# Kernel tuning notes

Hardware: AMD Instinct MI355X
Metric: run time of the kernel (lower is better)

Reference implementation:

```python
import jax, jax.numpy as jnp
import numpy as np

WIN = 32            # window_size
LOW_TH, HIGH_TH = 5.0, 15.0  # density_thresholds


def _prelu(x, a):
    return jnp.where(x >= 0, x, a * x)


def _hist_density(x):
    B, _, N = x.shape
    i, q = x[:, 0], x[:, 1]
    scale = WIN / 4.0  # bins over range [-2, 2]
    ii = jnp.clip(jnp.floor((i + 2.0) * scale).astype(jnp.int32), 0, WIN - 1)
    qq = jnp.clip(jnp.floor((q + 2.0) * scale).astype(jnp.int32), 0, WIN - 1)
    valid = (i >= -2.0) & (i <= 2.0) & (q >= -2.0) & (q <= 2.0)
    boff = jnp.arange(B, dtype=jnp.int32)[:, None] * (WIN * WIN)
    flat = (boff + ii * WIN + qq).reshape(-1)
    H = jax.ops.segment_sum(valid.astype(jnp.float32).reshape(-1), flat,
                            num_segments=B * WIN * WIN).reshape(B, WIN, WIN)
    low = (H <= LOW_TH).astype(jnp.float32)
    med = ((H > LOW_TH) & (H <= HIGH_TH)).astype(jnp.float32)
    high = (H > HIGH_TH).astype(jnp.float32)
    return jnp.stack([high, med, low], axis=1)


def _conv(x, w, b, p):
    y = jax.lax.conv_general_dilated(x, w, (1, 1), [(p, p), (p, p)],
                                     dimension_numbers=('NCHW', 'OIHW', 'NCHW'))
    return y + b[None, :, None, None]


def _avgpool2(x):
    B, C, H, W = x.shape
    return x.reshape(B, C, H // 2, 2, W // 2, 2).mean(axis=(3, 5))


def setup_inputs():
    key = jax.random.key(0)
    ks = jax.random.split(key, 8)
    B, N = 4096, 1024
    x = jax.random.normal(ks[0], (B, 2, N), jnp.float32)

    def w(k, shape, fan_in):
        return jax.random.normal(k, shape, jnp.float32) * (1.0 / np.sqrt(fan_in))

    return {
        'x': x,
        'cw1': w(ks[1], (32, 3, 3, 3), 3 * 9),   'cb1': jnp.zeros(32, jnp.float32),  'a1': jnp.float32(0.25),
        'cw2': w(ks[2], (64, 32, 3, 3), 32 * 9),  'cb2': jnp.zeros(64, jnp.float32),  'a2': jnp.float32(0.25),
        'cw3': w(ks[3], (128, 64, 5, 5), 64 * 25),'cb3': jnp.zeros(128, jnp.float32), 'a3': jnp.float32(0.25),
        'fw1': w(ks[4], (256, 128 * 4 * 4), 128 * 4 * 4), 'fb1': jnp.zeros(256, jnp.float32), 'a4': jnp.float32(0.25),
        'fw2': w(ks[5], (128, 256), 256), 'fb2': jnp.zeros(128, jnp.float32),
    }


def reference(x, cw1, cb1, a1, cw2, cb2, a2, cw3, cb3, a3, fw1, fb1, a4, fw2, fb2):
    d = _hist_density(x)                              # [B, 3, 32, 32]
    h = _avgpool2(_prelu(_conv(d, cw1, cb1, 1), a1))  # [B, 32, 16, 16]
    h = _avgpool2(_prelu(_conv(h, cw2, cb2, 1), a2))  # [B, 64, 8, 8]
    h = _avgpool2(_prelu(_conv(h, cw3, cb3, 2), a3))  # [B, 128, 4, 4]
    # AdaptiveAvgPool2d((4,4)) is identity on 4x4; Dropout is identity in eval
    f = h.reshape(h.shape[0], -1)                     # [B, 2048]
    f = _prelu(f @ fw1.T + fb1, a4)                   # [B, 256]
    return f @ fw2.T + fb2                            # [B, 128]
```

## Files before the change

kernel.cpp:

```cpp
#include <hip/hip_runtime.h>
#include <hip/hip_bf16.h>
#include <cstdint>
#include <cstddef>

typedef short short8 __attribute__((ext_vector_type(8)));
typedef float f32x4 __attribute__((ext_vector_type(4)));
typedef float f32x16 __attribute__((ext_vector_type(16)));
typedef unsigned short u16x4 __attribute__((ext_vector_type(4)));

__device__ inline unsigned short f2b(float f) {
    union { __hip_bfloat16 h; unsigned short u; } cv;
    cv.h = __float2bfloat16(f);
    return cv.u;
}
__device__ inline float b2f(unsigned short u) {
    union { __hip_bfloat16 h; unsigned short u; } cv;
    cv.u = u;
    return __bfloat162float(cv.h);
}
__device__ inline float prelu(float v, float a) { return v >= 0.f ? v : a * v; }

__global__ void k_prep(const float* __restrict__ cw1,
                       const float* __restrict__ cw2,
                       const float* __restrict__ cw3,
                       const float* __restrict__ fw1,
                       const float* __restrict__ fw2,
                       unsigned short* __restrict__ cw1e,
                       unsigned short* __restrict__ cw2bf,
                       unsigned short* __restrict__ cw3bf,
                       unsigned short* __restrict__ fw1hi,
                       unsigned short* __restrict__ fw1lo,
                       float* __restrict__ fw2t)
{
    const int i = blockIdx.x * 256 + threadIdx.x;
    const int stride = gridDim.x * 256;
    if (i < 1024) {
        const int oc = i >> 5, k = i & 31;
        float v = 0.f;
        if (k < 27) { const int tap = k / 3, c = k - 3 * tap; v = cw1[oc * 27 + c * 9 + tap]; }
        cw1e[i] = f2b(v);
    }
    if (i < 18432) {
        const int tap = i >> 11, r = i & 2047, oc = r >> 5, ic = r & 31;
        cw2bf[i] = f2b(cw2[oc * 288 + ic * 9 + tap]);
    }
    for (int j = i; j < 204800; j += stride) {
        const int tap = j >> 13, r = j & 8191, oc = r >> 6, ic = r & 63;
        cw3bf[j] = f2b(cw3[oc * 1600 + ic * 25 + tap]);
    }
    for (int j = i; j < 524288; j += stride) {
        const int oc = j >> 11, k = j & 2047;
        const float w = fw1[j];
        const unsigned short hi = f2b(w);
        const unsigned short lo = f2b(w - b2f(hi));
        const size_t o = ((size_t)(k >> 3) * 256 + oc) * 8 + (k & 7);
        fw1hi[o] = hi; fw1lo[o] = lo;
    }
    for (int j = i; j < 32768; j += stride) {
        const int k = j >> 7, oc = j & 127;
        fw2t[j] = fw2[oc * 256 + k];
    }
}

__global__ __launch_bounds__(256) void k_convstack(
    const float* __restrict__ x,
    const unsigned short* __restrict__ cw1e, const float* __restrict__ cb1, const float* __restrict__ a1p,
    const unsigned short* __restrict__ cw2bf, const float* __restrict__ cb2, const float* __restrict__ a2p,
    const unsigned short* __restrict__ cw3bf, const float* __restrict__ cb3, const float* __restrict__ a3p,
    unsigned short* __restrict__ h3out)
{
    const int b0 = blockIdx.x * 2;
    const int t = threadIdx.x;
    const int wv = t >> 6;
    const int l  = t & 63;
    const int lx = l & 15;
    const int q  = l >> 4;

    __shared__ unsigned char  clsp[1156];
    __shared__ unsigned short h1p[4 * 18 * 18 * 8];
    __shared__ unsigned short h2p[2][64 * 72];
    int* hist = (int*)(&h2p[1][0]);
    unsigned* umask = (unsigned*)(&h2p[1][2048]);

    const float a1 = *a1p, a2 = *a2p, a3 = *a3p;

    for (int i = t; i < 5184; i += 256) ((unsigned int*)h1p)[i] = 0u;

    for (int half = 0; half < 2; ++half) {
        const int b = b0 + half;

        for (int i = t; i < 1024; i += 256) hist[i] = 0;
        for (int i = t; i < 1156; i += 256) clsp[i] = 255;
        __syncthreads();

        const float* xb = x + (size_t)b * 2048;
        for (int n = t; n < 1024; n += 256) {
            const float iv = xb[n];
            const float qv = xb[1024 + n];
            if (iv >= -2.f && iv <= 2.f && qv >= -2.f && qv <= 2.f) {
                int ii = (int)floorf((iv + 2.f) * 8.f);
                int qq = (int)floorf((qv + 2.f) * 8.f);
                ii = ii < 0 ? 0 : (ii > 31 ? 31 : ii);
                qq = qq < 0 ? 0 : (qq > 31 ? 31 : qq);
                atomicAdd(&hist[ii * 32 + qq], 1);
            }
        }
        __syncthreads();

        for (int i = t; i < 1024; i += 256) {
            const int H = hist[i];
            clsp[(i >> 5) * 34 + (i & 31) + 35] = (H > 15) ? 0 : ((H > 5) ? 1 : 2);
        }
        __syncthreads();

        for (int i = t; i < 1024; i += 256) {
            const int y = i >> 5, xx = i & 31;
            unsigned m = 0;
            #pragma unroll
            for (int tap = 0; tap < 9; ++tap) {
                const int ky = tap / 3, kx = tap % 3;
                const unsigned c = clsp[(y + ky) * 34 + (xx + kx)];
                if (c < 3u) m |= 1u << (tap * 3 + c);
            }
            umask[i] = m;
        }
        __syncthreads();

        {
            const int mt = wv & 1;
            const int yh = wv >> 1;
            const short8 a1f = *(const short8*)(cw1e + (mt * 16 + lx) * 32 + q * 8);
            float b1r[4];
            #pragma unroll
            for (int r = 0; r < 4; ++r) b1r[r] = cb1[mt * 16 + q * 4 + r];

            for (int py = yh * 8; py < yh * 8 + 8; ++py) {
                f32x4 mac[4];
                #pragma unroll
                for (int d = 0; d < 4; ++d) {
                    const int y = 2 * py + (d >> 1);
                    const int xx = (d & 1) * 16 + lx;
                    const unsigned m = umask[y * 32 + xx];
                    short8 bf;
                    #pragma unroll
                    for (int j = 0; j < 8; ++j) {
                        const int k = q * 8 + j;
                        bf[j] = ((m >> k) & 1u) ? (short)0x3F80 : (short)0;
                    }
                    f32x4 z = {0.f, 0.f, 0.f, 0.f};
                    mac[d] = __builtin_amdgcn_mfma_f32_16x16x32_bf16(a1f, bf, z, 0, 0, 0);
                }
                #pragma unroll
                for (int hx = 0; hx < 2; ++hx) {
                    f32x4 u;
                    #pragma unroll
                    for (int r = 0; r < 4; ++r) {
                        float v0 = prelu(mac[hx][r] + b1r[r], a1);
                        float v1 = prelu(mac[2 + hx][r] + b1r[r], a1);
                        u[r] = v0 + v1;
                    }
                    #pragma unroll
                    for (int r = 0; r < 4; ++r) u[r] += __shfl_xor(u[r], 1);
                    if ((lx & 1) == 0) {
                        const int px = hx * 8 + (lx >> 1);
                        const int slot = mt * 2 + (q >> 1);
                        u16x4 pk;
                        #pragma unroll
                        for (int r = 0; r < 4; ++r) pk[r] = f2b(0.25f * u[r]);
                        *(u16x4*)(h1p + slot * 2592 + ((py + 1) * 18 + (px + 1)) * 8 + (q & 1) * 4) = pk;
                    }
                }
            }
        }
        __syncthreads();

        {
            short8 a2f[9];
            #pragma unroll
            for (int tap = 0; tap < 9; ++tap)
                a2f[tap] = *(const short8*)(cw2bf + tap * 2048 + (wv * 16 + lx) * 32 + q * 8);
            float b2r[4];
            #pragma unroll
            for (int r = 0; r < 4; ++r) b2r[r] = cb2[wv * 16 + q * 4 + r];

            for (int py = 0; py < 8; ++py) {
                f32x4 acc0 = {0.f, 0.f, 0.f, 0.f}, acc1 = {0.f, 0.f, 0.f, 0.f};
                const char* base0 = (const char*)h1p + q * 5184 + (2 * py * 18 + lx) * 16;
                const char* base1 = base0 + 288;
                #pragma unroll
                for (int tap = 0; tap < 9; ++tap) {
                    const int ky = tap / 3, kx = tap % 3;
                    const int imm = (ky * 18 + kx) * 16;
                    const short8 bf0 = *(const short8*)(base0 + imm);
                    acc0 = __builtin_amdgcn_mfma_f32_16x16x32_bf16(a2f[tap], bf0, acc0, 0, 0, 0);
                    const short8 bf1 = *(const short8*)(base1 + imm);
                    acc1 = __builtin_amdgcn_mfma_f32_16x16x32_bf16(a2f[tap], bf1, acc1, 0, 0, 0);
                }
                f32x4 u;
                #pragma unroll
                for (int r = 0; r < 4; ++r) {
                    float v0 = prelu(acc0[r] + b2r[r], a2);
                    float v1 = prelu(acc1[r] + b2r[r], a2);
                    u[r] = v0 + v1;
                }
                #pragma unroll
                for (int r = 0; r < 4; ++r) u[r] += __shfl_xor(u[r], 1);
                if ((lx & 1) == 0) {
                    const int pos = py * 8 + (lx >> 1);
                    u16x4 pk;
                    #pragma unroll
                    for (int r = 0; r < 4; ++r) pk[r] = f2b(0.25f * u[r]);
                    *(u16x4*)(&h2p[half][pos * 72 + wv * 16 + q * 4]) = pk;
                }
            }
        }
        __syncthreads();
    }

    {
        const int col = l & 31;
        const int hi  = l >> 5;

        f32x16 acc[4];
        #pragma unroll
        for (int nt = 0; nt < 4; ++nt)
            #pragma unroll
            for (int r = 0; r < 16; ++r) acc[nt][r] = 0.f;

        const unsigned short* abase = cw3bf + (size_t)(wv * 32 + col) * 64 + hi * 8;

        short8 aC[4], aN[4];
        #pragma unroll
        for (int kk = 0; kk < 4; ++kk)
            aC[kk] = *(const short8*)(abase + kk * 16);

        for (int tap = 0; tap < 25; ++tap) {
            if (tap < 24) {
                const unsigned short* anext = abase + (tap + 1) * 8192;
                #pragma unroll
                for (int kk = 0; kk < 4; ++kk)
                    aN[kk] = *(const short8*)(anext + kk * 16);
            }
            const int ky = (tap * 13) >> 6;
            const int kx = tap - 5 * ky;
            #pragma unroll
            for (int nt = 0; nt < 4; ++nt) {
                const int bb  = nt >> 1;
                const int pos = (nt & 1) * 32 + col;
                const int sy  = (pos >> 3) + ky - 2;
                const int sx  = (pos & 7) + kx - 2;
                const bool ok = (unsigned)sy < 8u && (unsigned)sx < 8u;
                const int soff = (sy * 8 + sx) * 72 + hi * 8;
                #pragma unroll
                for (int kk = 0; kk < 4; ++kk) {
                    short8 bf = {0, 0, 0, 0, 0, 0, 0, 0};
                    if (ok) bf = *(const short8*)(&h2p[bb][soff + kk * 16]);
                    acc[nt] = __builtin_amdgcn_mfma_f32_32x32x16_bf16(aC[kk], bf, acc[nt], 0, 0, 0);
                }
            }
            #pragma unroll
            for (int kk = 0; kk < 4; ++kk) aC[kk] = aN[kk];
        }

        float b3r[16];
        #pragma unroll
        for (int r = 0; r < 16; ++r)
            b3r[r] = cb3[wv * 32 + (r & 3) + 8 * (r >> 2) + 4 * hi];

        #pragma unroll
        for (int nt = 0; nt < 4; ++nt) {
            f32x16 u;
            #pragma unroll
            for (int r = 0; r < 16; ++r) u[r] = prelu(acc[nt][r] + b3r[r], a3);
            #pragma unroll
            for (int r = 0; r < 16; ++r) u[r] += __shfl_xor(u[r], 1);
            #pragma unroll
            for (int r = 0; r < 16; ++r) u[r] += __shfl_xor(u[r], 8);
            if ((col & 9) == 0) {
                const int b  = b0 + (nt >> 1);
                const int oy = (nt & 1) * 2 + (col >> 4);
                const int ox = (col & 7) >> 1;
                #pragma unroll
                for (int r = 0; r < 16; ++r) {
                    const int oc = wv * 32 + (r & 3) + 8 * (r >> 2) + 4 * hi;
                    h3out[(size_t)b * 2048 + oc * 16 + oy * 4 + ox] = f2b(0.25f * u[r]);
                }
            }
        }
    }
}

__global__ __launch_bounds__(512) void k_fc(
    const unsigned short* __restrict__ fw1hi,
    const unsigned short* __restrict__ fw1lo,
    const unsigned short* __restrict__ h3,
    const float* __restrict__ fb1, const float* __restrict__ a4p,
    const float* __restrict__ fw2t, const float* __restrict__ fb2,
    float* __restrict__ out)
{
    const int t  = threadIdx.x;
    const int wv = t >> 6;
    const int l  = t & 63;
    const int lx = l & 15;
    const int q  = l >> 4;
    const int b0 = blockIdx.x * 32;

    __shared__ unsigned short Bs[32 * 128];
    __shared__ float fT[256 * 34];

    f32x4 acc[2][2];
    #pragma unroll
    for (int mt = 0; mt < 2; ++mt)
        #pragma unroll
        for (int bn = 0; bn < 2; ++bn) { f32x4 z = {0.f,0.f,0.f,0.f}; acc[mt][bn] = z; }

    const int srow  = t >> 4;
    const int scolb = (t & 15) << 4;
    const unsigned short* gsrc = h3 + (size_t)(b0 + srow) * 2048
                               + ((scolb ^ ((srow & 7) << 4)) >> 1);

    for (int kc = 0; kc < 2048; kc += 128) {
        __builtin_amdgcn_global_load_lds(
            (const __attribute__((address_space(1))) unsigned int*)(gsrc + kc),
            (__attribute__((address_space(3))) unsigned int*)(Bs + t * 8),
            16, 0, 0);
        __syncthreads();

        #pragma unroll
        for (int s = 0; s < 4; ++s) {
            const int kb = ((kc + s * 32) >> 3) + q;
            const short8 ah0 = *(const short8*)(fw1hi + ((size_t)kb * 256 + wv * 32 + lx) * 8);
            const short8 ah1 = *(const short8*)(fw1hi + ((size_t)kb * 256 + wv * 32 + 16 + lx) * 8);
            const short8 al0 = *(const short8*)(fw1lo + ((size_t)kb * 256 + wv * 32 + lx) * 8);
            const short8 al1 = *(const short8*)(fw1lo + ((size_t)kb * 256 + wv * 32 + 16 + lx) * 8);
            #pragma unroll
            for (int bn = 0; bn < 2; ++bn) {
                const int rr = bn * 16 + lx;
                const short8 bfr = *(const short8*)((const char*)Bs + rr * 256
                                    + ((s * 64 + q * 16) ^ ((rr & 7) << 4)));
                acc[0][bn] = __builtin_amdgcn_mfma_f32_16x16x32_bf16(ah0, bfr, acc[0][bn], 0, 0, 0);
                acc[1][bn] = __builtin_amdgcn_mfma_f32_16x16x32_bf16(ah1, bfr, acc[1][bn], 0, 0, 0);
                acc[0][bn] = __builtin_amdgcn_mfma_f32_16x16x32_bf16(al0, bfr, acc[0][bn], 0, 0, 0);
                acc[1][bn] = __builtin_amdgcn_mfma_f32_16x16x32_bf16(al1, bfr, acc[1][bn], 0, 0, 0);
            }
        }
        __syncthreads();
    }

    const float a4 = *a4p;
    #pragma unroll
    for (int mt = 0; mt < 2; ++mt) {
        #pragma unroll
        for (int r = 0; r < 4; ++r) {
            const int oc = wv * 32 + mt * 16 + q * 4 + r;
            const float bb2 = fb1[oc];
            #pragma unroll
            for (int bn = 0; bn < 2; ++bn) {
                float v = acc[mt][bn][r] + bb2;
                v = v >= 0.f ? v : a4 * v;
                fT[oc * 34 + bn * 16 + lx] = v;
            }
        }
    }
    __syncthreads();

    {
        const int oc2 = t & 127;
        const int bh  = t >> 7;
        float acc2[8];
        #pragma unroll
        for (int j = 0; j < 8; ++j) acc2[j] = 0.f;
        for (int k = 0; k < 256; ++k) {
            const float w = fw2t[k * 128 + oc2];
            const float* fr = &fT[k * 34 + bh * 8];
            #pragma unroll
            for (int j = 0; j < 8; ++j) acc2[j] += w * fr[j];
        }
        const float bb2 = fb2[oc2];
        #pragma unroll
        for (int j = 0; j < 8; ++j)
            out[(size_t)(b0 + bh * 8 + j) * 128 + oc2] = acc2[j] + bb2;
    }
}

extern "C" void kernel_launch(void* const* d_in, const int* in_sizes, int n_in,
                              void* d_out, int out_size, void* d_ws, size_t ws_size,
                              hipStream_t stream)
{
    const float* x   = (const float*)d_in[0];
    const float* cw1 = (const float*)d_in[1];
    const float* cb1 = (const float*)d_in[2];
    const float* a1  = (const float*)d_in[3];
    const float* cw2 = (const float*)d_in[4];
    const float* cb2 = (const float*)d_in[5];
    const float* a2  = (const float*)d_in[6];
    const float* cw3 = (const float*)d_in[7];
    const float* cb3 = (const float*)d_in[8];
    const float* a3  = (const float*)d_in[9];
    const float* fw1 = (const float*)d_in[10];
    const float* fb1 = (const float*)d_in[11];
    const float* a4  = (const float*)d_in[12];
    const float* fw2 = (const float*)d_in[13];
    const float* fb2 = (const float*)d_in[14];
    float* out = (float*)d_out;

    unsigned short* cw1e  = (unsigned short*)((char*)d_ws);
    unsigned short* cw2bf = (unsigned short*)((char*)d_ws + 2048);
    unsigned short* cw3bf = (unsigned short*)((char*)d_ws + 38912);
    unsigned short* fw1hi = (unsigned short*)((char*)d_ws + 448512);
    unsigned short* fw1lo = (unsigned short*)((char*)d_ws + 1497088);
    float*          fw2t  = (float*)((char*)d_ws + 2545664);
    unsigned short* h3    = (unsigned short*)((char*)d_ws + 2676736);

    const int B = in_sizes[0] / 2048;

    k_prep<<<800, 256, 0, stream>>>(cw1, cw2, cw3, fw1, fw2,
                                    cw1e, cw2bf, cw3bf, fw1hi, fw1lo, fw2t);
    k_convstack<<<B / 2, 256, 0, stream>>>(x, cw1e, cb1, a1, cw2bf, cb2, a2,
                                           cw3bf, cb3, a3, h3);
    k_fc<<<B / 32, 512, 0, stream>>>(fw1hi, fw1lo, h3, fb1, a4, fw2t, fb2, out);
}
```

Before: 281.7 us.

## Pad conv2 output in LDS, run conv3 per sample, drop mask stage

The conv2 output is now written into a zero-padded, channel-slotted LDS layout, so the 5x5 conv3 reads need no bounds checks. Conv3 runs inside the per-sample loop, so the two-sample h2p buffer goes away. The separate umask pass and its barrier are removed: conv1 B fragments are built directly from the class map using precomputed tap offsets and class values. The histogram now aliases h1p, which needs a partial border re-zero each sample. In exchange each conv3 pass has only two independent accumulators instead of four, which reduces MFMA parallelism.

```diff
diff --git a/kernel.cpp b/kernel.cpp
--- a/kernel.cpp
+++ b/kernel.cpp
@@ -78,13 +78,24 @@
 
     __shared__ unsigned char  clsp[1156];
     __shared__ unsigned short h1p[4 * 18 * 18 * 8];
-    __shared__ unsigned short h2p[2][64 * 72];
-    int* hist = (int*)(&h2p[1][0]);
-    unsigned* umask = (unsigned*)(&h2p[1][2048]);
+    __shared__ unsigned short h2p[8 * 12 * 12 * 8];
+    int* hist = (int*)h1p;
 
     const float a1 = *a1p, a2 = *a2p, a3 = *a3p;
 
     for (int i = t; i < 5184; i += 256) ((unsigned int*)h1p)[i] = 0u;
+    for (int i = t; i < 4608; i += 256) ((unsigned int*)h2p)[i] = 0u;
+
+    int off1[8]; int cval[8];
+    #pragma unroll
+    for (int j = 0; j < 8; ++j) {
+        const int k = q * 8 + j;
+        const int tap = (k * 43) >> 7;
+        const int c   = k - 3 * tap;
+        const int ky  = (tap * 43) >> 7, kx = tap - 3 * ky;
+        off1[j] = ky * 34 + kx;
+        cval[j] = (k < 27) ? c : 200;
+    }
 
     for (int half = 0; half < 2; ++half) {
         const int b = b0 + half;
@@ -113,18 +124,13 @@
         }
         __syncthreads();
 
-        for (int i = t; i < 1024; i += 256) {
-            const int y = i >> 5, xx = i & 31;
-            unsigned m = 0;
-            #pragma unroll
-            for (int tap = 0; tap < 9; ++tap) {
-                const int ky = tap / 3, kx = tap % 3;
-                const unsigned c = clsp[(y + ky) * 34 + (xx + kx)];
-                if (c < 3u) m |= 1u << (tap * 3 + c);
-            }
-            umask[i] = m;
-        }
-        __syncthreads();
+        for (int p = t; p < 256; p += 256) {
+            const int r = p / 18, c = p - 18 * r;
+            if (r == 0 || c == 0 || c == 17) {
+                unsigned int* d = (unsigned int*)(h1p + p * 8);
+                d[0] = 0u; d[1] = 0u; d[2] = 0u; d[3] = 0u;
+            }
+        }
 
         {
             const int mt = wv & 1;
@@ -140,13 +146,11 @@
                 for (int d = 0; d < 4; ++d) {
                     const int y = 2 * py + (d >> 1);
                     const int xx = (d & 1) * 16 + lx;
-                    const unsigned m = umask[y * 32 + xx];
+                    const int pix = y * 34 + xx + 35;
                     short8 bf;
                     #pragma unroll
-                    for (int j = 0; j < 8; ++j) {
-                        const int k = q * 8 + j;
-                        bf[j] = ((m >> k) & 1u) ? (short)0x3F80 : (short)0;
-                    }
+                    for (int j = 0; j < 8; ++j)
+                        bf[j] = ((int)clsp[pix + off1[j] - 35] == cval[j]) ? (short)0x3F80 : (short)0;
                     f32x4 z = {0.f, 0.f, 0.f, 0.f};
                     mac[d] = __builtin_amdgcn_mfma_f32_16x16x32_bf16(a1f, bf, z, 0, 0, 0);
                 }
@@ -206,87 +210,90 @@
                 #pragma unroll
                 for (int r = 0; r < 4; ++r) u[r] += __shfl_xor(u[r], 1);
                 if ((lx & 1) == 0) {
-                    const int pos = py * 8 + (lx >> 1);
+                    const int px = lx >> 1;
+                    const int slot = wv * 2 + (q >> 1);
                     u16x4 pk;
                     #pragma unroll
                     for (int r = 0; r < 4; ++r) pk[r] = f2b(0.25f * u[r]);
-                    *(u16x4*)(&h2p[half][pos * 72 + wv * 16 + q * 4]) = pk;
-                }
-            }
-        }
-        __syncthreads();
-    }
-
-    {
-        const int col = l & 31;
-        const int hi  = l >> 5;
-
-        f32x16 acc[4];
-        #pragma unroll
-        for (int nt = 0; nt < 4; ++nt)
-            #pragma unroll
-            for (int r = 0; r < 16; ++r) acc[nt][r] = 0.f;
-
-        const unsigned short* abase = cw3bf + (size_t)(wv * 32 + col) * 64 + hi * 8;
-
-        short8 aC[4], aN[4];
-        #pragma unroll
-        for (int kk = 0; kk < 4; ++kk)
-            aC[kk] = *(const short8*)(abase + kk * 16);
-
-        for (int tap = 0; tap < 25; ++tap) {
-            if (tap < 24) {
-                const unsigned short* anext = abase + (tap + 1) * 8192;
-                #pragma unroll
-                for (int kk = 0; kk < 4; ++kk)
-                    aN[kk] = *(const short8*)(anext + kk * 16);
-            }
-            const int ky = (tap * 13) >> 6;
-            const int kx = tap - 5 * ky;
-            #pragma unroll
-            for (int nt = 0; nt < 4; ++nt) {
-                const int bb  = nt >> 1;
-                const int pos = (nt & 1) * 32 + col;
-                const int sy  = (pos >> 3) + ky - 2;
-                const int sx  = (pos & 7) + kx - 2;
-                const bool ok = (unsigned)sy < 8u && (unsigned)sx < 8u;
-                const int soff = (sy * 8 + sx) * 72 + hi * 8;
-                #pragma unroll
-                for (int kk = 0; kk < 4; ++kk) {
-                    short8 bf = {0, 0, 0, 0, 0, 0, 0, 0};
-                    if (ok) bf = *(const short8*)(&h2p[bb][soff + kk * 16]);
-                    acc[nt] = __builtin_amdgcn_mfma_f32_32x32x16_bf16(aC[kk], bf, acc[nt], 0, 0, 0);
-                }
-            }
-            #pragma unroll
-            for (int kk = 0; kk < 4; ++kk) aC[kk] = aN[kk];
-        }
-
-        float b3r[16];
-        #pragma unroll
-        for (int r = 0; r < 16; ++r)
-            b3r[r] = cb3[wv * 32 + (r & 3) + 8 * (r >> 2) + 4 * hi];
-
-        #pragma unroll
-        for (int nt = 0; nt < 4; ++nt) {
-            f32x16 u;
-            #pragma unroll
-            for (int r = 0; r < 16; ++r) u[r] = prelu(acc[nt][r] + b3r[r], a3);
-            #pragma unroll
-            for (int r = 0; r < 16; ++r) u[r] += __shfl_xor(u[r], 1);
-            #pragma unroll
-            for (int r = 0; r < 16; ++r) u[r] += __shfl_xor(u[r], 8);
-            if ((col & 9) == 0) {
-                const int b  = b0 + (nt >> 1);
-                const int oy = (nt & 1) * 2 + (col >> 4);
-                const int ox = (col & 7) >> 1;
-                #pragma unroll
-                for (int r = 0; r < 16; ++r) {
-                    const int oc = wv * 32 + (r & 3) + 8 * (r >> 2) + 4 * hi;
-                    h3out[(size_t)b * 2048 + oc * 16 + oy * 4 + ox] = f2b(0.25f * u[r]);
-                }
-            }
-        }
+                    *(u16x4*)(h2p + slot * 1152 + ((py + 2) * 12 + (px + 2)) * 8 + (q & 1) * 4) = pk;
+                }
+            }
+        }
+        __syncthreads();
+
+        {
+            const int col = l & 31;
+            const int hi  = l >> 5;
+            const int ry  = col >> 3;
+            const int rx  = col & 7;
+
+            f32x16 acc[2];
+            #pragma unroll
+            for (int nt = 0; nt < 2; ++nt)
+                #pragma unroll
+                for (int r = 0; r < 16; ++r) acc[nt][r] = 0.f;
+
+            const unsigned short* abase = cw3bf + (size_t)(wv * 32 + col) * 64 + hi * 8;
+            const char* bbase[2];
+            #pragma unroll
+            for (int nt = 0; nt < 2; ++nt) {
+                const int row = nt * 4 + ry;
+                bbase[nt] = (const char*)h2p + hi * 2304 + (row * 12 + rx) * 16;
+            }
+
+            short8 aC[4], aN[4];
+            #pragma unroll
+            for (int kk = 0; kk < 4; ++kk)
+                aC[kk] = *(const short8*)(abase + kk * 16);
+
+            for (int tap = 0; tap < 25; ++tap) {
+                if (tap < 24) {
+                    const unsigned short* anext = abase + (tap + 1) * 8192;
+                    #pragma unroll
+                    for (int kk = 0; kk < 4; ++kk)
+                        aN[kk] = *(const short8*)(anext + kk * 16);
+                }
+                const int ky = (tap * 13) >> 6;
+                const int kx = tap - 5 * ky;
+                const int imm = (ky * 12 + kx) * 16;
+                #pragma unroll
+                for (int nt = 0; nt < 2; ++nt) {
+                    #pragma unroll
+                    for (int kk = 0; kk < 4; ++kk) {
+                        const short8 bf = *(const short8*)(bbase[nt] + kk * 4608 + imm);
+                        acc[nt] = __builtin_amdgcn_mfma_f32_32x32x16_bf16(aC[kk], bf, acc[nt], 0, 0, 0);
+                    }
+                }
+                #pragma unroll
+                for (int kk = 0; kk < 4; ++kk) aC[kk] = aN[kk];
+            }
+
+            float b3r[16];
+            #pragma unroll
+            for (int r = 0; r < 16; ++r)
+                b3r[r] = cb3[wv * 32 + (r & 3) + 8 * (r >> 2) + 4 * hi];
+
+            #pragma unroll
+            for (int nt = 0; nt < 2; ++nt) {
+                f32x16 u;
+                #pragma unroll
+                for (int r = 0; r < 16; ++r) u[r] = prelu(acc[nt][r] + b3r[r], a3);
+                #pragma unroll
+                for (int r = 0; r < 16; ++r) u[r] += __shfl_xor(u[r], 1);
+                #pragma unroll
+                for (int r = 0; r < 16; ++r) u[r] += __shfl_xor(u[r], 8);
+                if ((col & 9) == 0) {
+                    const int oy = nt * 2 + (col >> 4);
+                    const int ox = (col & 7) >> 1;
+                    #pragma unroll
+                    for (int r = 0; r < 16; ++r) {
+                        const int oc = wv * 32 + (r & 3) + 8 * (r >> 2) + 4 * hi;
+                        h3out[(size_t)b * 2048 + oc * 16 + oy * 4 + ox] = f2b(0.25f * u[r]);
+                    }
+                }
+            }
+        }
+        __syncthreads();
     }
 }
 
```

Measured after the change: 561.9 us. 1.99x slower.

## Remap conv2 to 32x32x16 MFMA tiles with spatial-per-wave split and weight prefetch

Applied to the files above, without the earlier changes.

Conv2 is restructured so each wave computes all 64 output channels for two output rows using 32x32x16 bf16 MFMAs, instead of a 16-channel slice over all rows with 16x16x32 MFMAs. Weight fragments are streamed per tap from global or L2 with a one-tap-ahead prefetch, replacing the nine preloaded fragments. Activation fragments loaded from LDS are reused across two M tiles, and pooling uses cross-lane shuffles. This trades register pressure (four f32x16 accumulators) and per-tap weight loads for fewer LDS reads and larger MFMA instructions.

```diff
diff --git a/kernel.cpp b/kernel.cpp
--- a/kernel.cpp
+++ b/kernel.cpp
@@ -175,42 +175,88 @@
         __syncthreads();
 
         {
-            short8 a2f[9];
-            #pragma unroll
-            for (int tap = 0; tap < 9; ++tap)
-                a2f[tap] = *(const short8*)(cw2bf + tap * 2048 + (wv * 16 + lx) * 32 + q * 8);
-            float b2r[4];
-            #pragma unroll
-            for (int r = 0; r < 4; ++r) b2r[r] = cb2[wv * 16 + q * 4 + r];
-
-            for (int py = 0; py < 8; ++py) {
-                f32x4 acc0 = {0.f, 0.f, 0.f, 0.f}, acc1 = {0.f, 0.f, 0.f, 0.f};
-                const char* base0 = (const char*)h1p + q * 5184 + (2 * py * 18 + lx) * 16;
-                const char* base1 = base0 + 288;
-                #pragma unroll
-                for (int tap = 0; tap < 9; ++tap) {
-                    const int ky = tap / 3, kx = tap % 3;
-                    const int imm = (ky * 18 + kx) * 16;
-                    const short8 bf0 = *(const short8*)(base0 + imm);
-                    acc0 = __builtin_amdgcn_mfma_f32_16x16x32_bf16(a2f[tap], bf0, acc0, 0, 0, 0);
-                    const short8 bf1 = *(const short8*)(base1 + imm);
-                    acc1 = __builtin_amdgcn_mfma_f32_16x16x32_bf16(a2f[tap], bf1, acc1, 0, 0, 0);
-                }
-                f32x4 u;
-                #pragma unroll
-                for (int r = 0; r < 4; ++r) {
-                    float v0 = prelu(acc0[r] + b2r[r], a2);
-                    float v1 = prelu(acc1[r] + b2r[r], a2);
-                    u[r] = v0 + v1;
-                }
-                #pragma unroll
-                for (int r = 0; r < 4; ++r) u[r] += __shfl_xor(u[r], 1);
-                if ((lx & 1) == 0) {
-                    const int pos = py * 8 + (lx >> 1);
-                    u16x4 pk;
-                    #pragma unroll
-                    for (int r = 0; r < 4; ++r) pk[r] = f2b(0.25f * u[r]);
-                    *(u16x4*)(&h2p[half][pos * 72 + wv * 16 + q * 4]) = pk;
+            const int col = l & 31;
+            const int hi  = l >> 5;
+
+            f32x16 acc[2][2];
+            #pragma unroll
+            for (int mt = 0; mt < 2; ++mt)
+                #pragma unroll
+                for (int nt = 0; nt < 2; ++nt)
+                    #pragma unroll
+                    for (int r = 0; r < 16; ++r) acc[mt][nt][r] = 0.f;
+
+            const char* bb[2];
+            #pragma unroll
+            for (int nt = 0; nt < 2; ++nt) {
+                const int y0 = (wv * 2 + nt) * 2 + (col >> 4);
+                const int x0 = col & 15;
+                bb[nt] = (const char*)h1p + hi * 5184 + (y0 * 18 + x0) * 16;
+            }
+
+            const unsigned short* abase2 = cw2bf + col * 32 + hi * 8;
+
+            short8 aC[2][2], aN[2][2];
+            #pragma unroll
+            for (int mt = 0; mt < 2; ++mt)
+                #pragma unroll
+                for (int kk = 0; kk < 2; ++kk)
+                    aC[mt][kk] = *(const short8*)(abase2 + mt * 1024 + kk * 16);
+
+            #pragma unroll
+            for (int tap = 0; tap < 9; ++tap) {
+                if (tap < 8) {
+                    const unsigned short* anext = abase2 + (tap + 1) * 2048;
+                    #pragma unroll
+                    for (int mt = 0; mt < 2; ++mt)
+                        #pragma unroll
+                        for (int kk = 0; kk < 2; ++kk)
+                            aN[mt][kk] = *(const short8*)(anext + mt * 1024 + kk * 16);
+                }
+                const int ky = tap / 3, kx = tap % 3;
+                const int imm = (ky * 18 + kx) * 16;
+                #pragma unroll
+                for (int nt = 0; nt < 2; ++nt) {
+                    #pragma unroll
+                    for (int kk = 0; kk < 2; ++kk) {
+                        const short8 bf = *(const short8*)(bb[nt] + kk * 10368 + imm);
+                        acc[0][nt] = __builtin_amdgcn_mfma_f32_32x32x16_bf16(aC[0][kk], bf, acc[0][nt], 0, 0, 0);
+                        acc[1][nt] = __builtin_amdgcn_mfma_f32_32x32x16_bf16(aC[1][kk], bf, acc[1][nt], 0, 0, 0);
+                    }
+                }
+                #pragma unroll
+                for (int mt = 0; mt < 2; ++mt)
+                    #pragma unroll
+                    for (int kk = 0; kk < 2; ++kk) aC[mt][kk] = aN[mt][kk];
+            }
+
+            #pragma unroll
+            for (int mt = 0; mt < 2; ++mt) {
+                float b2r[16];
+                #pragma unroll
+                for (int r = 0; r < 16; ++r)
+                    b2r[r] = cb2[mt * 32 + (r & 3) + 8 * (r >> 2) + 4 * hi];
+                #pragma unroll
+                for (int nt = 0; nt < 2; ++nt) {
+                    f32x16 u;
+                    #pragma unroll
+                    for (int r = 0; r < 16; ++r) u[r] = prelu(acc[mt][nt][r] + b2r[r], a2);
+                    #pragma unroll
+                    for (int r = 0; r < 16; ++r) u[r] += __shfl_xor(u[r], 16);
+                    #pragma unroll
+                    for (int r = 0; r < 16; ++r) u[r] += __shfl_xor(u[r], 1);
+                    if ((col & 17) == 0) {
+                        const int py = wv * 2 + nt;
+                        const int px = (col & 15) >> 1;
+                        const int pos = py * 8 + px;
+                        #pragma unroll
+                        for (int g4 = 0; g4 < 4; ++g4) {
+                            u16x4 pk;
+                            #pragma unroll
+                            for (int r = 0; r < 4; ++r) pk[r] = f2b(0.25f * u[g4 * 4 + r]);
+                            *(u16x4*)(&h2p[half][pos * 72 + mt * 32 + 8 * g4 + 4 * hi]) = pk;
+                        }
+                    }
                 }
             }
         }
```

After: 454.3 us. +61.3%, slower.
